# Kernel optimization log

Hardware: AMD Instinct MI355X
Metric: run time of the kernel (lower is better)

## Reference

```python
import jax, jax.numpy as jnp
import numpy as np

N = 50000      # nodes (spots)
E = 800000     # edges (avg degree 16)
G = 1002       # num_genes + 2
D = 256        # latent_dim
C = 20         # num_celltypes
BN_EPS = 1e-5


def setup_inputs() -> dict:
    key = jax.random.key(0)
    ks = jax.random.split(key, 14)
    def p(k, shape, fan_in):
        return (jax.random.normal(k, shape, jnp.float32) / np.sqrt(fan_in)).astype(jnp.float32)
    return {
        "x": jax.random.normal(ks[0], (N, G), jnp.float32),
        "edge_index": jax.random.randint(ks[1], (2, E), 0, N, jnp.int64),
        "lin_w": p(ks[2], (G, D), G),          # encoder Linear (no bias)
        "conv1_w": p(ks[3], (D, D), D),
        "conv1_b": jnp.zeros((D,), jnp.float32),
        "conv2_w": p(ks[4], (D, D), D),
        "conv2_b": jnp.zeros((D,), jnp.float32),
        "mlp1_w": p(ks[5], (D, D), D),
        "mlp1_b": jnp.zeros((D,), jnp.float32),
        "bn_gamma": jnp.ones((D,), jnp.float32),
        "bn_beta": jnp.zeros((D,), jnp.float32),
        "mlp2_w": p(ks[6], (D, C), D),
        "mlp2_b": jnp.zeros((C,), jnp.float32),
    }


def _gcn_conv(x, src, dst, W, b):
    # x: [N, D]; symmetric GCN normalization with self-loops (weight 1)
    n = x.shape[0]
    x = x @ W
    deg = jax.ops.segment_sum(jnp.ones(src.shape[0], x.dtype), dst, num_segments=n) + 1.0
    dinv = jax.lax.rsqrt(deg)
    norm = dinv[src] * dinv[dst]                 # [E]
    agg = jax.ops.segment_sum(norm[:, None] * x[src], dst, num_segments=n)
    agg = agg + x * (1.0 / deg)[:, None]         # self-loop term: deg^-1 * x_i
    return agg + b


def reference(x, edge_index, lin_w, conv1_w, conv1_b, conv2_w, conv2_b,
              mlp1_w, mlp1_b, bn_gamma, bn_beta, mlp2_w, mlp2_b):
    src, dst = edge_index[0], edge_index[1]
    # encoder
    h = x @ lin_w
    h = jax.nn.relu(_gcn_conv(h, src, dst, conv1_w, conv1_b))
    h = jax.nn.relu(_gcn_conv(h, src, dst, conv2_w, conv2_b))
    # decoder MLP (Linear -> BatchNorm(train) -> ReLU -> Linear) + softmax
    h = h @ mlp1_w + mlp1_b
    mu = jnp.mean(h, axis=0)
    var = jnp.var(h, axis=0)
    h = (h - mu) * jax.lax.rsqrt(var + BN_EPS) * bn_gamma + bn_beta
    h = jax.nn.relu(h)
    h = h @ mlp2_w + mlp2_b
    return jax.nn.softmax(h, axis=-1)
```

## Files before the change

### kernel.cpp

```cpp
#include <hip/hip_runtime.h>
#include <cstdint>
#include <cstddef>

typedef unsigned short u16;
typedef unsigned int   u32;
typedef _Float16       f16;
typedef u16  u16x4 __attribute__((ext_vector_type(4)));
typedef u16  u16x8 __attribute__((ext_vector_type(8)));
typedef f16  f16x8 __attribute__((ext_vector_type(8)));
typedef float f32x4 __attribute__((ext_vector_type(4)));

static __device__ __forceinline__ u16 f2h(float f){
  f16 h = (f16)f;
  return __builtin_bit_cast(u16, h);
}
static __device__ __forceinline__ float h2f(u16 b){
  f16 h = __builtin_bit_cast(f16, b);
  return (float)h;
}

static __device__ __forceinline__ void async16(void* lds, const void* g){
  __builtin_amdgcn_global_load_lds(
      (const __attribute__((address_space(1))) u32*)g,
      (__attribute__((address_space(3))) u32*)lds, 16, 0, 0);
}

__global__ void transpose_weights(const float* __restrict__ lw, const float* __restrict__ w1,
                                  const float* __restrict__ w2, const float* __restrict__ w3,
                                  u16* __restrict__ lwT, u16* __restrict__ w1T,
                                  u16* __restrict__ w2T, u16* __restrict__ w3T,
                                  int G, int Gpad)
{
  __shared__ float t[32][33];
  int z = blockIdx.z;
  const float* in = (z==0)? lw : (z==1)? w1 : (z==2)? w2 : w3;
  u16* out        = (z==0)? lwT: (z==1)? w1T: (z==2)? w2T: w3T;
  int R   = (z==0)? G : 256;
  int ldo = (z==0)? Gpad : 256;
  int by = blockIdx.y, bx = blockIdx.x;
  if (by*32 >= R && z != 0) return;
  int tid = threadIdx.x;
  #pragma unroll
  for (int k=0;k<4;k++){
    int p = tid + k*256; int r = p>>5, c = p&31;
    int gr = by*32 + r;
    t[r][c] = (gr < R) ? in[gr*256 + bx*32 + c] : 0.f;
  }
  __syncthreads();
  #pragma unroll
  for (int k=0;k<4;k++){
    int p = tid + k*256; int r = p>>5, c = p&31;
    int oc = by*32 + c;
    if (oc < ldo) out[(bx*32 + r)*ldo + oc] = f2h(t[c][r]);
  }
}

__global__ void count_kernel(const int* __restrict__ dst, int* __restrict__ cnt, int E){
  int e = blockIdx.x*256 + threadIdx.x;
  if (e < E) atomicAdd(&cnt[dst[e]], 1);
}

__global__ void scan_reduce(const int* __restrict__ cnt, int* __restrict__ bsum, int N){
  __shared__ int s[256];
  int tid = threadIdx.x;
  int i = blockIdx.x*256 + tid;
  s[tid] = (i<N)? cnt[i] : 0;
  __syncthreads();
  for (int off=128; off>0; off>>=1){
    if (tid < off) s[tid] += s[tid+off];
    __syncthreads();
  }
  if (tid==0) bsum[blockIdx.x] = s[0];
}

__global__ void scan_offsets(const int* __restrict__ bsum, int* __restrict__ boff, int nb){
  __shared__ int s[256];
  int tid = threadIdx.x;
  int v = (tid<nb)? bsum[tid] : 0;
  s[tid] = v; __syncthreads();
  for (int off=1; off<256; off<<=1){
    int t = (tid>=off)? s[tid-off] : 0;
    __syncthreads();
    s[tid] += t;
    __syncthreads();
  }
  if (tid<nb) boff[tid] = s[tid]-v;
}

__global__ void scan_final(const int* __restrict__ cnt, const int* __restrict__ boff,
                           int* __restrict__ row_ptr, float* __restrict__ dinv, int N, int E){
  __shared__ int s[256];
  int tid = threadIdx.x;
  int i = blockIdx.x*256 + tid;
  int v = (i<N)? cnt[i] : 0;
  s[tid] = v; __syncthreads();
  for (int off=1; off<256; off<<=1){
    int t = (tid>=off)? s[tid-off] : 0;
    __syncthreads();
    s[tid] += t;
    __syncthreads();
  }
  if (i < N){
    row_ptr[i] = boff[blockIdx.x] + s[tid] - v;
    dinv[i] = rsqrtf((float)(v+1));
  }
  if (i == N-1) row_ptr[N] = E;
}

__global__ void scatter_kernel(const int* __restrict__ src, const int* __restrict__ dst,
                               const int* __restrict__ row_ptr, int* __restrict__ cursor,
                               int* __restrict__ colx, int E){
  int e = blockIdx.x*256 + threadIdx.x;
  if (e < E){
    int d = dst[e];
    int pos = atomicAdd(&cursor[d], 1);
    colx[row_ptr[d] + pos] = src[e];
  }
}

template<bool XPATH, bool ADD_BIAS>
__global__ __launch_bounds__(256) void gemm_async(
    const void* __restrict__ Av, int lda, int Ka,
    const u16* __restrict__ BT, int Kpad,
    u16* __restrict__ C, const float* __restrict__ bias, int M)
{
  __shared__ __align__(16) char AsRaw[XPATH ? 16384 : 8192];
  __shared__ __align__(16) u16  Bs[128*32];
  float* Asf = (float*)AsRaw;
  u16*   Ash = (u16*)AsRaw;

  const int tid  = threadIdx.x;
  const int lane = tid & 63;
  const int quad = lane >> 4;
  const int l16  = lane & 15;
  const int wave = tid >> 6;
  const int wm = (wave >> 1) << 6;
  const int wn = (wave & 1) << 6;
  const int m0 = blockIdx.y << 7;
  const int n0 = blockIdx.x << 7;

  const u16* bg[2];
  u16* lB[2];
  #pragma unroll
  for (int i=0;i<2;i++){
    int q = wave*2 + i;
    int rr = lane >> 2, ss = lane & 3;
    int gg = ss ^ ((rr >> 1) & 3);
    bg[i] = BT + (size_t)(n0 + q*16 + rr)*Kpad + gg*8;
    lB[i] = Bs + q*512;
  }

  const float* agf[4]; u16* lAf[4];
  const u16*   agh[2]; u16* lAh[2];
  if constexpr (XPATH){
    const float* Af = (const float*)Av;
    #pragma unroll
    for (int i=0;i<4;i++){
      int q = wave*4 + i;
      int rr = lane >> 3, ss = lane & 7;
      int gg = ss ^ rr;
      int gr = m0 + q*8 + rr;
      if (gr >= M) gr = M-1;
      agf[i] = Af + (size_t)gr*lda + gg*4;
      lAf[i] = (u16*)(Asf + q*256);
    }
  } else {
    const u16* Ah = (const u16*)Av;
    #pragma unroll
    for (int i=0;i<2;i++){
      int q = wave*2 + i;
      int rr = lane >> 2, ss = lane & 3;
      int gg = ss ^ ((rr >> 1) & 3);
      int gr = m0 + q*16 + rr;
      if (gr >= M) gr = M-1;
      agh[i] = Ah + (size_t)gr*lda + gg*8;
      lAh[i] = Ash + q*512;
    }
  }

  f32x4 acc[4][4];
  #pragma unroll
  for (int i=0;i<4;i++)
    #pragma unroll
    for (int j=0;j<4;j++) acc[i][j] = {0.f,0.f,0.f,0.f};

  for (int k0 = 0; k0 < Kpad; k0 += 32){
    bool tail = XPATH && (k0 + 32 > Ka);
    #pragma unroll
    for (int i=0;i<2;i++) async16(lB[i], bg[i] + k0);
    if constexpr (XPATH){
      if (!tail){
        #pragma unroll
        for (int i=0;i<4;i++) async16(lAf[i], agf[i] + k0);
      } else {
        const float* Af = (const float*)Av;
        int row = tid >> 1, half = tid & 1;
        int gr = m0 + row;
        bool rv = gr < M;
        #pragma unroll
        for (int g2=0; g2<4; g2++){
          int g = half*4 + g2;
          int slot = g ^ (row & 7);
          float* dst = Asf + row*32 + slot*4;
          #pragma unroll
          for (int c=0;c<4;c++){
            int gc = k0 + g*4 + c;
            dst[c] = (rv && gc < Ka) ? Af[(size_t)gr*lda + gc] : 0.f;
          }
        }
      }
    } else {
      #pragma unroll
      for (int i=0;i<2;i++) async16(lAh[i], agh[i] + k0);
    }
    asm volatile("s_waitcnt vmcnt(0)" ::: "memory");
    __syncthreads();

    f16x8 af[4], bf[4];
    if constexpr (XPATH){
      #pragma unroll
      for (int mt=0;mt<4;mt++){
        int R = wm + mt*16 + l16;
        const float* rb = Asf + R*32;
        int x7 = R & 7;
        int s0 = (quad*2)   ^ x7;
        int s1 = (quad*2+1) ^ x7;
        f32x4 lo = *(const f32x4*)(rb + s0*4);
        f32x4 hi = *(const f32x4*)(rb + s1*4);
        union { f16x8 v; u32 w[4]; } u;
        u.w[0] = __builtin_bit_cast(u32, __builtin_amdgcn_cvt_pkrtz(lo[0], lo[1]));
        u.w[1] = __builtin_bit_cast(u32, __builtin_amdgcn_cvt_pkrtz(lo[2], lo[3]));
        u.w[2] = __builtin_bit_cast(u32, __builtin_amdgcn_cvt_pkrtz(hi[0], hi[1]));
        u.w[3] = __builtin_bit_cast(u32, __builtin_amdgcn_cvt_pkrtz(hi[2], hi[3]));
        af[mt] = u.v;
      }
    } else {
      #pragma unroll
      for (int mt=0;mt<4;mt++){
        int R = wm + mt*16 + l16;
        int s = quad ^ ((R >> 1) & 3);
        af[mt] = __builtin_bit_cast(f16x8, *(const u16x8*)(Ash + R*32 + s*8));
      }
    }
    #pragma unroll
    for (int nt=0;nt<4;nt++){
      int R = wn + nt*16 + l16;
      int s = quad ^ ((R >> 1) & 3);
      bf[nt] = __builtin_bit_cast(f16x8, *(const u16x8*)(Bs + R*32 + s*8));
    }
    #pragma unroll
    for (int mt=0;mt<4;mt++)
      #pragma unroll
      for (int nt=0;nt<4;nt++)
        acc[mt][nt] = __builtin_amdgcn_mfma_f32_16x16x32_f16(af[mt], bf[nt], acc[mt][nt], 0, 0, 0);
    __syncthreads();
  }

  #pragma unroll
  for (int mt=0;mt<4;mt++){
    #pragma unroll
    for (int nt=0;nt<4;nt++){
      int col = n0 + wn + nt*16 + l16;
      float bv = 0.f;
      if constexpr (ADD_BIAS) bv = bias[col];
      #pragma unroll
      for (int r=0;r<4;r++){
        int row = m0 + wm + mt*16 + quad*4 + r;
        if (row < M) C[(size_t)row*256 + col] = f2h(acc[mt][nt][r] + bv);
      }
    }
  }
}

__global__ __launch_bounds__(256) void agg_kernel(
    const u16* __restrict__ XW, const float* __restrict__ bias,
    const float* __restrict__ dinv, const int* __restrict__ row_ptr,
    const int* __restrict__ colx, u16* __restrict__ H, int N)
{
  int wid = (blockIdx.x << 2) + (threadIdx.x >> 6);
  if (wid >= N) return;
  int lane = threadIdx.x & 63;
  int f = lane << 2;
  float di = dinv[wid];
  int e0 = row_ptr[wid], e1 = row_ptr[wid+1];
  int deg = e1 - e0;
  float a0=0.f, a1=0.f, a2=0.f, a3=0.f;
  for (int base = 0; base < deg; base += 64){
    int mi = 0;
    if (base + lane < deg) mi = colx[e0 + base + lane];
    int cnt = min(deg - base, 64);
    int j = 0;
    for (; j+1 < cnt; j += 2){
      int s0 = __shfl(mi, j);
      int s1 = __shfl(mi, j+1);
      float w0 = dinv[s0]*di;
      float w1 = dinv[s1]*di;
      u16x4 x0 = *(const u16x4*)(XW + (size_t)s0*256 + f);
      u16x4 x1 = *(const u16x4*)(XW + (size_t)s1*256 + f);
      a0 += w0*h2f(x0[0]) + w1*h2f(x1[0]);
      a1 += w0*h2f(x0[1]) + w1*h2f(x1[1]);
      a2 += w0*h2f(x0[2]) + w1*h2f(x1[2]);
      a3 += w0*h2f(x0[3]) + w1*h2f(x1[3]);
    }
    if (j < cnt){
      int s0 = __shfl(mi, j);
      float w0 = dinv[s0]*di;
      u16x4 x0 = *(const u16x4*)(XW + (size_t)s0*256 + f);
      a0 += w0*h2f(x0[0]); a1 += w0*h2f(x0[1]);
      a2 += w0*h2f(x0[2]); a3 += w0*h2f(x0[3]);
    }
  }
  u16x4 xs = *(const u16x4*)(XW + (size_t)wid*256 + f);
  float wd = di*di;
  a0 += wd*h2f(xs[0]); a1 += wd*h2f(xs[1]); a2 += wd*h2f(xs[2]); a3 += wd*h2f(xs[3]);
  const float4 bb = *(const float4*)(bias + f);
  a0 = fmaxf(a0 + bb.x, 0.f);
  a1 = fmaxf(a1 + bb.y, 0.f);
  a2 = fmaxf(a2 + bb.z, 0.f);
  a3 = fmaxf(a3 + bb.w, 0.f);
  u16x4 o = { f2h(a0), f2h(a1), f2h(a2), f2h(a3) };
  *(u16x4*)(H + (size_t)wid*256 + f) = o;
}

__global__ void bn_stats(const u16* __restrict__ H, float* __restrict__ bsum,
                         float* __restrict__ bsq, int N){
  int col = threadIdx.x;
  float s=0.f, q=0.f;
  for (int r=blockIdx.x; r<N; r+=gridDim.x){
    float v = h2f(H[(size_t)r*256 + col]);
    s += v; q += v*v;
  }
  atomicAdd(&bsum[col], s);
  atomicAdd(&bsq[col], q);
}

__global__ void bn_finalize(const float* __restrict__ bsum, const float* __restrict__ bsq,
                            const float* __restrict__ gamma, const float* __restrict__ beta,
                            float* __restrict__ scale, float* __restrict__ shift, int N){
  int c = threadIdx.x;
  float invN = 1.f/(float)N;
  float mu  = bsum[c]*invN;
  float var = bsq[c]*invN - mu*mu;
  float sc  = gamma[c] * rsqrtf(var + 1e-5f);
  scale[c] = sc;
  shift[c] = beta[c] - mu*sc;
}

__global__ __launch_bounds__(256) void final_kernel(
    const u16* __restrict__ H, const float* __restrict__ scale, const float* __restrict__ shift,
    const float* __restrict__ W2, const float* __restrict__ b2, float* __restrict__ out, int N)
{
  __shared__ float W2s[256*20];
  __shared__ float scs[256];
  __shared__ float shs[256];
  __shared__ float b2s[20];
  int tid = threadIdx.x;
  for (int i=tid; i<5120; i+=256) W2s[i] = W2[i];
  scs[tid] = scale[tid];
  shs[tid] = shift[tid];
  if (tid < 20) b2s[tid] = b2[tid];
  __syncthreads();
  int r = blockIdx.x*256 + tid;
  if (r >= N) return;
  float l[20];
  #pragma unroll
  for (int c=0;c<20;c++) l[c] = b2s[c];
  const u16* hrow = H + (size_t)r*256;
  for (int j0=0;j0<256;j0+=8){
    u16x8 h8 = *(const u16x8*)(hrow + j0);
    #pragma unroll
    for (int t=0;t<8;t++){
      int j = j0+t;
      float a = fmaxf(fmaf(h2f(h8[t]), scs[j], shs[j]), 0.f);
      const float* wr = W2s + j*20;
      #pragma unroll
      for (int c=0;c<20;c++) l[c] = fmaf(a, wr[c], l[c]);
    }
  }
  float m = l[0];
  #pragma unroll
  for (int c=1;c<20;c++) m = fmaxf(m, l[c]);
  float ssum = 0.f;
  #pragma unroll
  for (int c=0;c<20;c++){ l[c] = __expf(l[c]-m); ssum += l[c]; }
  float inv = 1.f/ssum;
  float* orow = out + (size_t)r*20;
  #pragma unroll
  for (int c=0;c<20;c++) orow[c] = l[c]*inv;
}

extern "C" void kernel_launch(void* const* d_in, const int* in_sizes, int n_in,
                              void* d_out, int out_size, void* d_ws, size_t ws_size,
                              hipStream_t stream)
{
  (void)n_in; (void)out_size; (void)ws_size;
  const float* x     = (const float*)d_in[0];
  const int*   ei    = (const int*)d_in[1];
  const float* lin_w = (const float*)d_in[2];
  const float* c1w   = (const float*)d_in[3];
  const float* c1b   = (const float*)d_in[4];
  const float* c2w   = (const float*)d_in[5];
  const float* c2b   = (const float*)d_in[6];
  const float* m1w   = (const float*)d_in[7];
  const float* m1b   = (const float*)d_in[8];
  const float* gam   = (const float*)d_in[9];
  const float* bet   = (const float*)d_in[10];
  const float* m2w   = (const float*)d_in[11];
  const float* m2b   = (const float*)d_in[12];
  float* out = (float*)d_out;

  const int E = in_sizes[1]/2;
  const int G = in_sizes[2]/256;
  const int N = in_sizes[0]/G;
  const int Gpad = (G + 31) & ~31;
  const int* srcI = ei;
  const int* dstI = ei + E;

  char* w = (char*)d_ws;
  auto alloc = [&](size_t bytes)->char*{
    char* p = w;
    w += (bytes + 255) & ~(size_t)255;
    return p;
  };
  u16* Ha    = (u16*)alloc((size_t)N*256*2);
  u16* Hb    = (u16*)alloc((size_t)N*256*2);
  u16* linT  = (u16*)alloc((size_t)256*Gpad*2);
  u16* w1T   = (u16*)alloc(256*256*2);
  u16* w2T   = (u16*)alloc(256*256*2);
  u16* w3T   = (u16*)alloc(256*256*2);
  int* cnt    = (int*)alloc((size_t)N*4);
  int* cursor = (int*)alloc((size_t)N*4);
  int* rowp   = (int*)alloc((size_t)(N+1)*4);
  int* colx   = (int*)alloc((size_t)E*4);
  float* dinv = (float*)alloc((size_t)N*4);
  int* bsum   = (int*)alloc(1024);
  int* boff   = (int*)alloc(1024);
  float* bnsum= (float*)alloc(1024);
  float* bnsq = (float*)alloc(1024);
  float* scl  = (float*)alloc(1024);
  float* shf  = (float*)alloc(1024);

  hipMemsetAsync(cnt,    0, (size_t)N*4, stream);
  hipMemsetAsync(cursor, 0, (size_t)N*4, stream);
  hipMemsetAsync(bnsum,  0, 2048, stream);

  const int NB = (N + 255)/256;

  transpose_weights<<<dim3(8, Gpad>>5, 4), 256, 0, stream>>>(
      lin_w, c1w, c2w, m1w, linT, w1T, w2T, w3T, G, Gpad);
  count_kernel  <<<dim3((E+255)/256), 256, 0, stream>>>(dstI, cnt, E);
  scan_reduce   <<<dim3(NB), 256, 0, stream>>>(cnt, bsum, N);
  scan_offsets  <<<dim3(1),  256, 0, stream>>>(bsum, boff, NB);
  scan_final    <<<dim3(NB), 256, 0, stream>>>(cnt, boff, rowp, dinv, N, E);
  scatter_kernel<<<dim3((E+255)/256), 256, 0, stream>>>(srcI, dstI, rowp, cursor, colx, E);

  dim3 ggrid(2, (N+127)/128);
  gemm_async<true,  false><<<ggrid, 256, 0, stream>>>(x,  G,   G,   linT, Gpad, Ha, nullptr, N);
  gemm_async<false, false><<<ggrid, 256, 0, stream>>>(Ha, 256, 256, w1T,  256,  Hb, nullptr, N);
  agg_kernel<<<dim3((N+3)/4), 256, 0, stream>>>(Hb, c1b, dinv, rowp, colx, Ha, N);
  gemm_async<false, false><<<ggrid, 256, 0, stream>>>(Ha, 256, 256, w2T,  256,  Hb, nullptr, N);
  agg_kernel<<<dim3((N+3)/4), 256, 0, stream>>>(Hb, c2b, dinv, rowp, colx, Ha, N);
  gemm_async<false, true ><<<ggrid, 256, 0, stream>>>(Ha, 256, 256, w3T,  256,  Hb, m1b, N);
  bn_stats   <<<dim3(256), 256, 0, stream>>>(Hb, bnsum, bnsq, N);
  bn_finalize<<<dim3(1),   256, 0, stream>>>(bnsum, bnsq, gam, bet, scl, shf, N);
  final_kernel<<<dim3(NB), 256, 0, stream>>>(Hb, scl, shf, m2w, m2b, out, N);
}
```

Before: 726.1 us.

## Double-buffer LDS tiles in gemm_async to overlap global loads with MFMA

The GEMM kernel now keeps two LDS buffers for the A and B tiles and issues the async global-to-LDS loads for the next K step before computing on the current one. Partial vmcnt waits let the current tile's loads be consumed while the next tile's loads are still in flight, with the manual zero-padded tail load handled as its own stage. The aim is to hide global memory latency, which previously sat exposed behind a full vmcnt(0) wait on every iteration. In exchange the kernel uses twice the LDS, which can lower occupancy, and it depends on exact vmcnt counts matching the number of async loads issued per stage.

```diff
diff --git a/kernel.cpp b/kernel.cpp
--- a/kernel.cpp
+++ b/kernel.cpp
@@ -124,10 +124,8 @@
     const u16* __restrict__ BT, int Kpad,
     u16* __restrict__ C, const float* __restrict__ bias, int M)
 {
-  __shared__ __align__(16) char AsRaw[XPATH ? 16384 : 8192];
-  __shared__ __align__(16) u16  Bs[128*32];
-  float* Asf = (float*)AsRaw;
-  u16*   Ash = (u16*)AsRaw;
+  __shared__ __align__(16) char AsRaw[2][XPATH ? 16384 : 8192];
+  __shared__ __align__(16) u16  Bs[2][128*32];
 
   const int tid  = threadIdx.x;
   const int lane = tid & 63;
@@ -139,6 +137,9 @@
   const int m0 = blockIdx.y << 7;
   const int n0 = blockIdx.x << 7;
 
+  const int ABUF = XPATH ? 8192 : 4096;
+  const int BBUF = 4096;
+
   const u16* bg[2];
   u16* lB[2];
   #pragma unroll
@@ -147,7 +148,7 @@
     int rr = lane >> 2, ss = lane & 3;
     int gg = ss ^ ((rr >> 1) & 3);
     bg[i] = BT + (size_t)(n0 + q*16 + rr)*Kpad + gg*8;
-    lB[i] = Bs + q*512;
+    lB[i] = &Bs[0][0] + q*512;
   }
 
   const float* agf[4]; u16* lAf[4];
@@ -162,7 +163,7 @@
       int gr = m0 + q*8 + rr;
       if (gr >= M) gr = M-1;
       agf[i] = Af + (size_t)gr*lda + gg*4;
-      lAf[i] = (u16*)(Asf + q*256);
+      lAf[i] = (u16*)&AsRaw[0][0] + q*512;
     }
   } else {
     const u16* Ah = (const u16*)Av;
@@ -174,9 +175,40 @@
       int gr = m0 + q*16 + rr;
       if (gr >= M) gr = M-1;
       agh[i] = Ah + (size_t)gr*lda + gg*8;
-      lAh[i] = Ash + q*512;
-    }
-  }
+      lAh[i] = (u16*)&AsRaw[0][0] + q*512;
+    }
+  }
+
+  auto stage_async = [&](int buf, int k0){
+    #pragma unroll
+    for (int i=0;i<2;i++) async16(lB[i] + buf*BBUF, bg[i] + k0);
+    if constexpr (XPATH){
+      #pragma unroll
+      for (int i=0;i<4;i++) async16(lAf[i] + buf*ABUF, agf[i] + k0);
+    } else {
+      #pragma unroll
+      for (int i=0;i<2;i++) async16(lAh[i] + buf*ABUF, agh[i] + k0);
+    }
+  };
+
+  auto stageA_manual = [&](int buf, int k0){
+    const float* Af = (const float*)Av;
+    float* AsfW = (float*)&AsRaw[buf][0];
+    int row = tid >> 1, half = tid & 1;
+    int gr = m0 + row;
+    bool rv = gr < M;
+    #pragma unroll
+    for (int g2=0; g2<4; g2++){
+      int g = half*4 + g2;
+      int slot = g ^ (row & 7);
+      float* dst = AsfW + row*32 + slot*4;
+      #pragma unroll
+      for (int c=0;c<4;c++){
+        int gc = k0 + g*4 + c;
+        dst[c] = (rv && gc < Ka) ? Af[(size_t)gr*lda + gc] : 0.f;
+      }
+    }
+  };
 
   f32x4 acc[4][4];
   #pragma unroll
@@ -184,44 +216,49 @@
     #pragma unroll
     for (int j=0;j<4;j++) acc[i][j] = {0.f,0.f,0.f,0.f};
 
-  for (int k0 = 0; k0 < Kpad; k0 += 32){
-    bool tail = XPATH && (k0 + 32 > Ka);
-    #pragma unroll
-    for (int i=0;i<2;i++) async16(lB[i], bg[i] + k0);
-    if constexpr (XPATH){
-      if (!tail){
+  const int NT = Kpad >> 5;
+  const int tailT = (XPATH && (Ka < Kpad)) ? NT-1 : NT;
+
+  if (XPATH && tailT == 0){
+    #pragma unroll
+    for (int i=0;i<2;i++) async16(lB[i], bg[i]);
+    stageA_manual(0, 0);
+  } else {
+    stage_async(0, 0);
+  }
+
+  int cur = 0;
+  for (int t=0; t<NT; ++t){
+    const bool have = (t+1) < NT;
+    const bool nman = XPATH && ((t+1) == tailT);
+    if (have){
+      const int k0n = (t+1) << 5;
+      if (nman){
         #pragma unroll
-        for (int i=0;i<4;i++) async16(lAf[i], agf[i] + k0);
+        for (int i=0;i<2;i++) async16(lB[i] + (cur^1)*BBUF, bg[i] + k0n);
+        stageA_manual(cur^1, k0n);
       } else {
-        const float* Af = (const float*)Av;
-        int row = tid >> 1, half = tid & 1;
-        int gr = m0 + row;
-        bool rv = gr < M;
-        #pragma unroll
-        for (int g2=0; g2<4; g2++){
-          int g = half*4 + g2;
-          int slot = g ^ (row & 7);
-          float* dst = Asf + row*32 + slot*4;
-          #pragma unroll
-          for (int c=0;c<4;c++){
-            int gc = k0 + g*4 + c;
-            dst[c] = (rv && gc < Ka) ? Af[(size_t)gr*lda + gc] : 0.f;
-          }
-        }
+        stage_async(cur^1, k0n);
       }
+    }
+    if (have && !nman){
+      if constexpr (XPATH) asm volatile("s_waitcnt vmcnt(6)" ::: "memory");
+      else                 asm volatile("s_waitcnt vmcnt(4)" ::: "memory");
     } else {
-      #pragma unroll
-      for (int i=0;i<2;i++) async16(lAh[i], agh[i] + k0);
-    }
-    asm volatile("s_waitcnt vmcnt(0)" ::: "memory");
-    __syncthreads();
+      asm volatile("s_waitcnt vmcnt(0) lgkmcnt(0)" ::: "memory");
+    }
+    __builtin_amdgcn_s_barrier();
+
+    const float* AsfC = (const float*)&AsRaw[cur][0];
+    const u16*   AshC = (const u16*)&AsRaw[cur][0];
+    const u16*   BsC  = &Bs[cur][0];
 
     f16x8 af[4], bf[4];
     if constexpr (XPATH){
       #pragma unroll
       for (int mt=0;mt<4;mt++){
         int R = wm + mt*16 + l16;
-        const float* rb = Asf + R*32;
+        const float* rb = AsfC + R*32;
         int x7 = R & 7;
         int s0 = (quad*2)   ^ x7;
         int s1 = (quad*2+1) ^ x7;
@@ -239,21 +276,23 @@
       for (int mt=0;mt<4;mt++){
         int R = wm + mt*16 + l16;
         int s = quad ^ ((R >> 1) & 3);
-        af[mt] = __builtin_bit_cast(f16x8, *(const u16x8*)(Ash + R*32 + s*8));
+        af[mt] = __builtin_bit_cast(f16x8, *(const u16x8*)(AshC + R*32 + s*8));
       }
     }
     #pragma unroll
     for (int nt=0;nt<4;nt++){
       int R = wn + nt*16 + l16;
       int s = quad ^ ((R >> 1) & 3);
-      bf[nt] = __builtin_bit_cast(f16x8, *(const u16x8*)(Bs + R*32 + s*8));
+      bf[nt] = __builtin_bit_cast(f16x8, *(const u16x8*)(BsC + R*32 + s*8));
     }
     #pragma unroll
     for (int mt=0;mt<4;mt++)
       #pragma unroll
       for (int nt=0;nt<4;nt++)
         acc[mt][nt] = __builtin_amdgcn_mfma_f32_16x16x32_f16(af[mt], bf[nt], acc[mt][nt], 0, 0, 0);
-    __syncthreads();
+
+    __builtin_amdgcn_s_barrier();
+    cur ^= 1;
   }
 
   #pragma unroll
```

After: 729.6 us. No clear change (+0.5%).

## Pre-pack x into fp16 tiled layout and double-buffer GEMM LDS staging

Applied to the files above, without the earlier changes.

Adds a pack_x kernel that converts the fp32 input x into fp16 laid out in pre-swizzled 128x32 tiles, so the first GEMM streams contiguous fp16 tiles with async LDS loads instead of loading fp32 and converting in the inner loop. The GEMM is also restructured into a two-stage double-buffered pipeline that prefetches the next K tile while computing the current one. The pack pass adds an extra full read of x (about 200MB) plus a write of roughly 100MB, and each GEMM block now needs twice the LDS for its A and B tiles, which may lower occupancy.

```diff
diff --git a/kernel.cpp b/kernel.cpp
--- a/kernel.cpp
+++ b/kernel.cpp
@@ -55,6 +55,37 @@
   }
 }
 
+__global__ __launch_bounds__(256) void pack_x(
+    const float* __restrict__ x, u16* __restrict__ P, int N, int G)
+{
+  int tid = threadIdx.x;
+  int r   = blockIdx.x*8 + (tid>>5);
+  int c8l = tid & 31;
+  int m = r >> 7, R = r & 127, q = R >> 4, rr = R & 15;
+  int sc = (rr >> 1) & 3;
+  bool rv = r < N;
+  const float* xr = x + (size_t)r*G;
+  #pragma unroll
+  for (int p=0;p<4;p++){
+    int c8 = c8l + p*32;
+    int c0 = c8*8;
+    u16x8 o;
+    #pragma unroll
+    for (int j=0;j<8;j+=2){
+      float2 v = {0.f, 0.f};
+      if (rv && (c0 + j + 1) < G)      v = *(const float2*)(xr + c0 + j);
+      else if (rv && (c0 + j) < G)     v.x = xr[c0 + j];
+      o[j]   = f2h(v.x);
+      o[j+1] = f2h(v.y);
+    }
+    int t  = c8 >> 2;
+    int gg = c8 & 3;
+    int ss = gg ^ sc;
+    int l  = rr*4 + ss;
+    *(u16x8*)(P + ((size_t)(m*32 + t))*4096 + q*512 + l*8) = o;
+  }
+}
+
 __global__ void count_kernel(const int* __restrict__ dst, int* __restrict__ cnt, int E){
   int e = blockIdx.x*256 + threadIdx.x;
   if (e < E) atomicAdd(&cnt[dst[e]], 1);
@@ -118,16 +149,14 @@
   }
 }
 
-template<bool XPATH, bool ADD_BIAS>
+template<bool APACKED, bool ADD_BIAS>
 __global__ __launch_bounds__(256) void gemm_async(
-    const void* __restrict__ Av, int lda, int Ka,
+    const u16* __restrict__ Ah, int lda,
     const u16* __restrict__ BT, int Kpad,
     u16* __restrict__ C, const float* __restrict__ bias, int M)
 {
-  __shared__ __align__(16) char AsRaw[XPATH ? 16384 : 8192];
-  __shared__ __align__(16) u16  Bs[128*32];
-  float* Asf = (float*)AsRaw;
-  u16*   Ash = (u16*)AsRaw;
+  __shared__ __align__(16) u16 As[2][4096];
+  __shared__ __align__(16) u16 Bs[2][4096];
 
   const int tid  = threadIdx.x;
   const int lane = tid & 63;
@@ -147,36 +176,34 @@
     int rr = lane >> 2, ss = lane & 3;
     int gg = ss ^ ((rr >> 1) & 3);
     bg[i] = BT + (size_t)(n0 + q*16 + rr)*Kpad + gg*8;
-    lB[i] = Bs + q*512;
-  }
-
-  const float* agf[4]; u16* lAf[4];
-  const u16*   agh[2]; u16* lAh[2];
-  if constexpr (XPATH){
-    const float* Af = (const float*)Av;
-    #pragma unroll
-    for (int i=0;i<4;i++){
-      int q = wave*4 + i;
-      int rr = lane >> 3, ss = lane & 7;
-      int gg = ss ^ rr;
-      int gr = m0 + q*8 + rr;
-      if (gr >= M) gr = M-1;
-      agf[i] = Af + (size_t)gr*lda + gg*4;
-      lAf[i] = (u16*)(Asf + q*256);
-    }
-  } else {
-    const u16* Ah = (const u16*)Av;
-    #pragma unroll
-    for (int i=0;i<2;i++){
-      int q = wave*2 + i;
+    lB[i] = &Bs[0][0] + q*512;
+  }
+
+  const u16* ag[2];
+  u16* lA[2];
+  #pragma unroll
+  for (int i=0;i<2;i++){
+    int q = wave*2 + i;
+    if constexpr (APACKED){
+      ag[i] = Ah + (size_t)blockIdx.y*32*4096 + q*512 + lane*8;
+    } else {
       int rr = lane >> 2, ss = lane & 3;
       int gg = ss ^ ((rr >> 1) & 3);
       int gr = m0 + q*16 + rr;
       if (gr >= M) gr = M-1;
-      agh[i] = Ah + (size_t)gr*lda + gg*8;
-      lAh[i] = Ash + q*512;
-    }
-  }
+      ag[i] = Ah + (size_t)gr*lda + gg*8;
+    }
+    lA[i] = &As[0][0] + q*512;
+  }
+
+  auto stage = [&](int buf, int t){
+    const int kb = t << 5;
+    #pragma unroll
+    for (int i=0;i<2;i++) async16(lB[i] + buf*4096, bg[i] + kb);
+    #pragma unroll
+    for (int i=0;i<2;i++)
+      async16(lA[i] + buf*4096, APACKED ? (ag[i] + (size_t)t*4096) : (ag[i] + kb));
+  };
 
   f32x4 acc[4][4];
   #pragma unroll
@@ -184,76 +211,43 @@
     #pragma unroll
     for (int j=0;j<4;j++) acc[i][j] = {0.f,0.f,0.f,0.f};
 
-  for (int k0 = 0; k0 < Kpad; k0 += 32){
-    bool tail = XPATH && (k0 + 32 > Ka);
-    #pragma unroll
-    for (int i=0;i<2;i++) async16(lB[i], bg[i] + k0);
-    if constexpr (XPATH){
-      if (!tail){
-        #pragma unroll
-        for (int i=0;i<4;i++) async16(lAf[i], agf[i] + k0);
-      } else {
-        const float* Af = (const float*)Av;
-        int row = tid >> 1, half = tid & 1;
-        int gr = m0 + row;
-        bool rv = gr < M;
-        #pragma unroll
-        for (int g2=0; g2<4; g2++){
-          int g = half*4 + g2;
-          int slot = g ^ (row & 7);
-          float* dst = Asf + row*32 + slot*4;
-          #pragma unroll
-          for (int c=0;c<4;c++){
-            int gc = k0 + g*4 + c;
-            dst[c] = (rv && gc < Ka) ? Af[(size_t)gr*lda + gc] : 0.f;
-          }
-        }
-      }
+  const int NT = Kpad >> 5;
+
+  stage(0, 0);
+  int cur = 0;
+  for (int t=0; t<NT; ++t){
+    if (t+1 < NT){
+      stage(cur^1, t+1);
+      asm volatile("s_waitcnt vmcnt(4)" ::: "memory");
     } else {
-      #pragma unroll
-      for (int i=0;i<2;i++) async16(lAh[i], agh[i] + k0);
-    }
-    asm volatile("s_waitcnt vmcnt(0)" ::: "memory");
-    __syncthreads();
+      asm volatile("s_waitcnt vmcnt(0)" ::: "memory");
+    }
+    __builtin_amdgcn_s_barrier();
+
+    const u16* AshC = &As[cur][0];
+    const u16* BsC  = &Bs[cur][0];
 
     f16x8 af[4], bf[4];
-    if constexpr (XPATH){
-      #pragma unroll
-      for (int mt=0;mt<4;mt++){
-        int R = wm + mt*16 + l16;
-        const float* rb = Asf + R*32;
-        int x7 = R & 7;
-        int s0 = (quad*2)   ^ x7;
-        int s1 = (quad*2+1) ^ x7;
-        f32x4 lo = *(const f32x4*)(rb + s0*4);
-        f32x4 hi = *(const f32x4*)(rb + s1*4);
-        union { f16x8 v; u32 w[4]; } u;
-        u.w[0] = __builtin_bit_cast(u32, __builtin_amdgcn_cvt_pkrtz(lo[0], lo[1]));
-        u.w[1] = __builtin_bit_cast(u32, __builtin_amdgcn_cvt_pkrtz(lo[2], lo[3]));
-        u.w[2] = __builtin_bit_cast(u32, __builtin_amdgcn_cvt_pkrtz(hi[0], hi[1]));
-        u.w[3] = __builtin_bit_cast(u32, __builtin_amdgcn_cvt_pkrtz(hi[2], hi[3]));
-        af[mt] = u.v;
-      }
-    } else {
-      #pragma unroll
-      for (int mt=0;mt<4;mt++){
-        int R = wm + mt*16 + l16;
-        int s = quad ^ ((R >> 1) & 3);
-        af[mt] = __builtin_bit_cast(f16x8, *(const u16x8*)(Ash + R*32 + s*8));
-      }
+    #pragma unroll
+    for (int mt=0;mt<4;mt++){
+      int R = wm + mt*16 + l16;
+      int s = quad ^ ((R >> 1) & 3);
+      af[mt] = __builtin_bit_cast(f16x8, *(const u16x8*)(AshC + R*32 + s*8));
     }
     #pragma unroll
     for (int nt=0;nt<4;nt++){
       int R = wn + nt*16 + l16;
       int s = quad ^ ((R >> 1) & 3);
-      bf[nt] = __builtin_bit_cast(f16x8, *(const u16x8*)(Bs + R*32 + s*8));
+      bf[nt] = __builtin_bit_cast(f16x8, *(const u16x8*)(BsC + R*32 + s*8));
     }
     #pragma unroll
     for (int mt=0;mt<4;mt++)
       #pragma unroll
       for (int nt=0;nt<4;nt++)
         acc[mt][nt] = __builtin_amdgcn_mfma_f32_16x16x32_f16(af[mt], bf[nt], acc[mt][nt], 0, 0, 0);
-    __syncthreads();
+
+    __builtin_amdgcn_s_barrier();
+    cur ^= 1;
   }
 
   #pragma unroll
@@ -413,6 +407,7 @@
   const int G = in_sizes[2]/256;
   const int N = in_sizes[0]/G;
   const int Gpad = (G + 31) & ~31;
+  const int MB128 = (N + 127) >> 7;
   const int* srcI = ei;
   const int* dstI = ei + E;
 
@@ -424,6 +419,7 @@
   };
   u16* Ha    = (u16*)alloc((size_t)N*256*2);
   u16* Hb    = (u16*)alloc((size_t)N*256*2);
+  u16* packA = (u16*)alloc((size_t)MB128*128*Gpad*2);
   u16* linT  = (u16*)alloc((size_t)256*Gpad*2);
   u16* w1T   = (u16*)alloc(256*256*2);
   u16* w2T   = (u16*)alloc(256*256*2);
@@ -448,19 +444,20 @@
 
   transpose_weights<<<dim3(8, Gpad>>5, 4), 256, 0, stream>>>(
       lin_w, c1w, c2w, m1w, linT, w1T, w2T, w3T, G, Gpad);
+  pack_x<<<dim3(MB128*16), 256, 0, stream>>>(x, packA, N, G);
   count_kernel  <<<dim3((E+255)/256), 256, 0, stream>>>(dstI, cnt, E);
   scan_reduce   <<<dim3(NB), 256, 0, stream>>>(cnt, bsum, N);
   scan_offsets  <<<dim3(1),  256, 0, stream>>>(bsum, boff, NB);
   scan_final    <<<dim3(NB), 256, 0, stream>>>(cnt, boff, rowp, dinv, N, E);
   scatter_kernel<<<dim3((E+255)/256), 256, 0, stream>>>(srcI, dstI, rowp, cursor, colx, E);
 
-  dim3 ggrid(2, (N+127)/128);
-  gemm_async<true,  false><<<ggrid, 256, 0, stream>>>(x,  G,   G,   linT, Gpad, Ha, nullptr, N);
-  gemm_async<false, false><<<ggrid, 256, 0, stream>>>(Ha, 256, 256, w1T,  256,  Hb, nullptr, N);
+  dim3 ggrid(2, MB128);
+  gemm_async<true,  false><<<ggrid, 256, 0, stream>>>(packA, 0,  linT, Gpad, Ha, nullptr, N);
+  gemm_async<false, false><<<ggrid, 256, 0, stream>>>(Ha, 256, w1T,  256,  Hb, nullptr, N);
   agg_kernel<<<dim3((N+3)/4), 256, 0, stream>>>(Hb, c1b, dinv, rowp, colx, Ha, N);
-  gemm_async<false, false><<<ggrid, 256, 0, stream>>>(Ha, 256, 256, w2T,  256,  Hb, nullptr, N);
+  gemm_async<false, false><<<ggrid, 256, 0, stream>>>(Ha, 256, w2T,  256,  Hb, nullptr, N);
   agg_kernel<<<dim3((N+3)/4), 256, 0, stream>>>(Hb, c2b, dinv, rowp, colx, Ha, N);
-  gemm_async<false, true ><<<ggrid, 256, 0, stream>>>(Ha, 256, 256, w3T,  256,  Hb, m1b, N);
+  gemm_async<false, true ><<<ggrid, 256, 0, stream>>>(Ha, 256, w3T,  256,  Hb, m1b, N);
   bn_stats   <<<dim3(256), 256, 0, stream>>>(Hb, bnsum, bnsq, N);
   bn_finalize<<<dim3(1),   256, 0, stream>>>(bnsum, bnsq, gam, bet, scl, shf, N);
   final_kernel<<<dim3(NB), 256, 0, stream>>>(Hb, scl, shf, m2w, m2b, out, N);
```

After: 752.4 us. 3.6% more time.
